# Kernel tuning notes

Hardware: AMD Instinct MI355X
Metric: run time of the kernel (lower is better)

## Reference

```python
import jax, jax.numpy as jnp
import numpy as np

DECAY = 0.2
TAU = float(-1.0 / np.log(DECAY))
THRESH = 0.5
DELAY = 0.1  # hidden spike events are scheduled at t + 0.1

B, E = 256, 1024
D_IN, D_H, D_OUT = 784, 400, 10
TIME_WINDOW = 64


def setup_inputs() -> dict:
    key = jax.random.key(0)
    k1, k2, k3, k4, k5, k6 = jax.random.split(key, 6)
    # chronologically sorted input spike event times per sample, in [0, time_window)
    event_times = jnp.sort(
        jax.random.uniform(k1, (B, E), dtype=jnp.float32) * TIME_WINDOW, axis=1
    )
    event_pixels = jax.random.randint(k2, (B, E), 0, D_IN, dtype=jnp.int32)
    W1 = jax.random.normal(k3, (D_H, D_IN), dtype=jnp.float32) * 0.1
    b1 = jax.random.normal(k4, (D_H,), dtype=jnp.float32) * 0.01
    W2 = jax.random.normal(k5, (D_OUT, D_H), dtype=jnp.float32) * 0.1
    b2 = jax.random.normal(k6, (D_OUT,), dtype=jnp.float32) * 0.01
    return {
        "event_times": event_times,
        "event_pixels": event_pixels,
        "W1": W1,
        "b1": b1,
        "W2": W2,
        "b2": b2,
        "time_window": TIME_WINDOW,
    }


def reference(event_times, event_pixels, W1, b1, W2, b2, time_window):
    # Event-driven LIF simulation, 784 -> 400 -> 10.
    # refractory_period == 0.0 in the source, so the refractory check never fires.
    Bn = event_times.shape[0]
    W1T = W1.T                               # [784, 400] for per-event gather
    bias1 = b1 / 784.0                       # bias contribution per input spike
    W2cols = W2.T + b2[None, :] / 400.0      # [400, 10] contribution per hidden spike
    tw = jnp.asarray(time_window, dtype=event_times.dtype)

    def hidden_event(carry, x):
        # Sequentially process one hidden neuron's (possible) spike within a
        # same-time group; resets can trigger mid-group so order matters.
        h2, counts = carry
        s, w = x                             # s: [B] bool, w: [10]
        mem_new = jnp.where(s[:, None], h2 + w[None, :], h2)
        f2 = s[:, None] & (mem_new >= THRESH)
        counts = counts + f2.astype(h2.dtype)
        h2 = jnp.where(f2, jnp.zeros_like(h2), mem_new)
        return (h2, counts), None

    def step(carry, x):
        h1, h2, counts, t1_prev, t2_prev = carry
        t, p = x                             # t: [B] float, p: [B] int
        # layer 1: decay to current time, integrate input spike, fire & reset
        h1 = h1 * jnp.exp(-(t - t1_prev) / TAU)[:, None] + W1T[p] + bias1[None, :]
        fired = h1 >= THRESH                 # [B, 400]
        h1 = jnp.where(fired, jnp.zeros_like(h1), h1)
        # layer 2: hidden events of this group all occur at t + DELAY
        th = t + DELAY
        h2 = h2 * jnp.exp(-(th - t2_prev) / TAU)[:, None]
        (h2, counts), _ = jax.lax.scan(hidden_event, (h2, counts), (fired.T, W2cols))
        return (h1, h2, counts, t, th), None

    f32 = event_times.dtype
    init = (
        jnp.zeros((Bn, 400), f32),           # h1_mem
        jnp.zeros((Bn, 10), f32),            # h2_mem
        jnp.zeros((Bn, 10), f32),            # h2_spike_counts
        jnp.zeros((Bn,), f32),               # h1 last update time
        jnp.zeros((Bn,), f32),               # h2 last update time
    )
    xs = (event_times.T, event_pixels.T)     # scan over E events chronologically
    (_, _, counts, _, _), _ = jax.lax.scan(step, init, xs)
    return counts / tw                       # [B, 10] rate-coded output
```

## Files before the change

### kernel.cpp

```cpp
#include <hip/hip_runtime.h>

#define CH 32
#define NCHUNK 32
#define NE 1024
#define DH 400
#define DIN 784
#define PF 8

#define TAUF ((float)0.6213349345596119)

__global__ void prep_transpose(const float* __restrict__ W1, float* __restrict__ W1T) {
  int idx = blockIdx.x * 256 + threadIdx.x;
  const int total = DIN * DH;
  if (idx < total) {
    int p = idx / DH;
    int j = idx - p * DH;
    W1T[idx] = W1[j * DIN + p];
  } else if (idx < total + 64) {
    W1T[idx] = 0.0f;
  }
}

#define STEP(WV)                                   \
  do {                                             \
    float mn_ = __fadd_rn(h2, (WV));               \
    bool f_ = (mn_ >= 0.5f);                       \
    cntf = f_ ? (cntf + 1.0f) : cntf;              \
    h2 = f_ ? 0.0f : mn_;                          \
  } while (0)

#define SPEC8(W0, W1, W2, W3, W4, W5, W6, W7)                                  \
  do {                                                                         \
    float q0f = __fadd_rn(h2, (W0));                                           \
    float q1f = __fadd_rn(q0f, (W1));                                          \
    float q2f = __fadd_rn(q1f, (W2));                                          \
    float q3f = __fadd_rn(q2f, (W3));                                          \
    float q4f = __fadd_rn(q3f, (W4));                                          \
    float q5f = __fadd_rn(q4f, (W5));                                          \
    float q6f = __fadd_rn(q5f, (W6));                                          \
    float q7f = __fadd_rn(q6f, (W7));                                          \
    bool anyF = (q0f >= 0.5f) | (q1f >= 0.5f) | (q2f >= 0.5f) | (q3f >= 0.5f) |\
                (q4f >= 0.5f) | (q5f >= 0.5f) | (q6f >= 0.5f) | (q7f >= 0.5f); \
    if (!anyF) {                                                               \
      h2 = q7f;                                                                \
    } else {                                                                   \
      STEP(W0); STEP(W1); STEP(W2); STEP(W3);                                  \
      STEP(W4); STEP(W5); STEP(W6); STEP(W7);                                  \
    }                                                                          \
  } while (0)

#define WSEL(PW, CW, WB)                            \
  do {                                              \
    bool c_ = (N >= (PW));                          \
    q = c_ ? (CW) : q;                              \
    r = c_ ? (N - (PW)) : r;                        \
    wb = c_ ? (WB) : wb;                            \
  } while (0)

#define RSEL64()                                                               \
  unsigned lo = (unsigned)q, hi = (unsigned)(q >> 32);                         \
  unsigned pc = (unsigned)__popc(lo);                                          \
  bool gg = r >= pc; unsigned base = gg ? 32u : 0u;                            \
  unsigned x = gg ? hi : lo; r = gg ? r - pc : r;                              \
  pc = (unsigned)__popc(x & 0xFFFFu); gg = r >= pc; base += gg ? 16u : 0u;     \
  x = gg ? (x >> 16) : (x & 0xFFFFu); r = gg ? r - pc : r;                     \
  pc = (unsigned)__popc(x & 0xFFu); gg = r >= pc; base += gg ? 8u : 0u;        \
  x = gg ? (x >> 8) : (x & 0xFFu); r = gg ? r - pc : r;                        \
  pc = (unsigned)__popc(x & 0xFu); gg = r >= pc; base += gg ? 4u : 0u;         \
  x = gg ? (x >> 4) : (x & 0xFu); r = gg ? r - pc : r;                         \
  pc = (unsigned)__popc(x & 0x3u); gg = r >= pc; base += gg ? 2u : 0u;         \
  x = gg ? (x >> 2) : (x & 0x3u); r = gg ? r - pc : r;                         \
  gg = r >= (x & 1u); base += gg ? 1u : 0u;

template <bool TR>
__global__ __launch_bounds__(512, 2) void snn_main(
    const float* __restrict__ ET, const int* __restrict__ EP,
    const float* __restrict__ W1x, const float* __restrict__ b1,
    const float* __restrict__ W2, const float* __restrict__ b2,
    float* __restrict__ out) {
  __shared__ float s_W2c[401 * 16];
  __shared__ unsigned long long s_masks[3][CH][8];
  __shared__ float s_dec1[NE];
  __shared__ float s_dec2[NE];
  __shared__ int s_EP[NE];
  __shared__ __align__(16) int s_spklist[2][CH][64];
  __shared__ float s_wlist[2][CH][256];
  __shared__ int s_spkcnt[2][CH];
  __shared__ __align__(16) int s_spk2[64];

  const int tid = threadIdx.x;
  const int b = blockIdx.x;
  const int eb = b * NE;

  for (int i = tid; i < 401 * 16; i += 512) {
    int row = i >> 4, col = i & 15;
    float v = 0.0f;
    if (row < DH && col < 10) v = __fadd_rn(W2[col * DH + row], __fdiv_rn(b2[col], 400.0f));
    s_W2c[i] = v;
  }
  for (int i = tid; i < NE; i += 512) {
    s_EP[i] = EP[eb + i];
    float t = ET[eb + i];
    float tp = (i > 0) ? ET[eb + i - 1] : 0.0f;
    s_dec1[i] = expf(__fdiv_rn(-(t - tp), TAUF));
    float th = __fadd_rn(t, 0.1f);
    float thp = (i > 0) ? __fadd_rn(tp, 0.1f) : 0.0f;
    s_dec2[i] = expf(__fdiv_rn(-(th - thp), TAUF));
  }

  const bool isProd = (tid < 448);
  const int lane = tid & 63;
  const int wv = tid >> 6;
  const bool act = (tid < DH);

  float m1 = 0.0f;
  float b1v = act ? __fdiv_rn(b1[tid < DH ? tid : DH - 1], 784.0f) : 0.0f;
  float wp[PF];
  int pnP[PF];

  float h2 = 0.0f, cntf = 0.0f;
  const int kk = lane & 15;

  __syncthreads();

  if (isProd) {
#pragma unroll
    for (int i = 0; i < PF; ++i) {
      int p = s_EP[i];
      wp[i] = TR ? W1x[p * DH + tid] : W1x[(tid < DH ? tid : DH - 1) * DIN + p];
      pnP[i] = s_EP[i + PF];
    }
  } else {
#pragma unroll
    for (int i = 0; i < PF; ++i) { wp[i] = 0.0f; pnP[i] = 0; }
  }

  for (int it = 0; it <= NCHUNK + 1; ++it) {
    if (isProd) {
      if (it < NCHUNK) {
        const int mb = it % 3;
        const int gbase = it * CH;
#pragma unroll
        for (int e = 0; e < CH; ++e) {
          const int g = gbase + e;
          const int s = e & (PF - 1);
          float mm = __fmul_rn(m1, s_dec1[g]);
          mm = __fadd_rn(mm, wp[s]);
          mm = __fadd_rn(mm, b1v);
          bool fired = act && (mm >= 0.5f);
          unsigned long long bal = __ballot(fired);
          m1 = fired ? 0.0f : mm;
          if (lane == 0) s_masks[mb][e][wv] = bal;
          int pn = pnP[s];
          wp[s] = TR ? W1x[pn * DH + tid] : W1x[(tid < DH ? tid : DH - 1) * DIN + pn];
          pnP[s] = s_EP[(g + 2 * PF) & (NE - 1)];
        }
      }
      if (it >= 1 && it <= NCHUNK) {
        const int c = it - 1;
        const int mb = c % 3;
        const int lb = c & 1;
        for (int e = wv; e < CH; e += 7) {
          unsigned long long c0 = s_masks[mb][e][0];
          unsigned long long c1 = s_masks[mb][e][1];
          unsigned long long c2 = s_masks[mb][e][2];
          unsigned long long c3 = s_masks[mb][e][3];
          unsigned long long c4 = s_masks[mb][e][4];
          unsigned long long c5 = s_masks[mb][e][5];
          unsigned long long c6 = s_masks[mb][e][6];
          unsigned P1 = (unsigned)__popcll(c0);
          unsigned P2 = P1 + (unsigned)__popcll(c1);
          unsigned P3 = P2 + (unsigned)__popcll(c2);
          unsigned P4 = P3 + (unsigned)__popcll(c3);
          unsigned P5 = P4 + (unsigned)__popcll(c4);
          unsigned P6 = P5 + (unsigned)__popcll(c5);
          unsigned total = P6 + (unsigned)__popcll(c6);
          unsigned N = (unsigned)lane;
          unsigned long long q = c0;
          unsigned r = N, wb = 0;
          WSEL(P1, c1, 64);  WSEL(P2, c2, 128); WSEL(P3, c3, 192);
          WSEL(P4, c4, 256); WSEL(P5, c5, 320); WSEL(P6, c6, 384);
          RSEL64();
          int j = (int)(wb + base);
          j = (N < total) ? j : DH;
          s_spklist[lb][e][lane] = j;
          if (lane == 0) s_spkcnt[lb][e] = (int)total;
#pragma unroll
          for (int p = 0; p < 4; ++p) {
            int sl = p * 4 + (lane >> 4);
            int js = __builtin_amdgcn_ds_bpermute(sl << 2, j);
            float w = s_W2c[js * 16 + (lane & 15)];
            s_wlist[lb][e][sl * 16 + (lane & 15)] = w;
          }
        }
      }
    } else {
      if (it >= 2) {
        const int c = it - 2;
        const int lb = c & 1;
        const int mb = c % 3;
        const int gb2 = c * CH;

        auto loadEvt = [&](int ee, int& tot, float& cdv, float (&w)[16]) {
          tot = s_spkcnt[lb][ee];
          cdv = s_dec2[gb2 + ee];
#pragma unroll
          for (int i = 0; i < 16; ++i) w[i] = s_wlist[lb][ee][i * 16 + kk];
        };
        auto procEvt = [&](int e, int tot, float cdv, float (&w)[16]) {
          h2 = __fmul_rn(h2, cdv);
          if (tot > 0) {
            SPEC8(w[0], w[1], w[2], w[3], w[4], w[5], w[6], w[7]);
            if (tot > 8) {
              SPEC8(w[8], w[9], w[10], w[11], w[12], w[13], w[14], w[15]);
            }
            if (tot > 16) {
              int lim = tot < 64 ? tot : 64;
              for (int dn = 16; dn < lim; dn += 8) {
                const int4* sp = (const int4*)(&s_spklist[lb][e][dn]);
                int4 ja = sp[0], jb = sp[1];
                float v0 = s_W2c[ja.x * 16 + kk];
                float v1 = s_W2c[ja.y * 16 + kk];
                float v2 = s_W2c[ja.z * 16 + kk];
                float v3 = s_W2c[ja.w * 16 + kk];
                float v4 = s_W2c[jb.x * 16 + kk];
                float v5 = s_W2c[jb.y * 16 + kk];
                float v6 = s_W2c[jb.z * 16 + kk];
                float v7 = s_W2c[jb.w * 16 + kk];
                SPEC8(v0, v1, v2, v3, v4, v5, v6, v7);
              }
              if (tot > 64) {
                unsigned long long c0 = s_masks[mb][e][0];
                unsigned long long c1 = s_masks[mb][e][1];
                unsigned long long c2 = s_masks[mb][e][2];
                unsigned long long c3 = s_masks[mb][e][3];
                unsigned long long c4 = s_masks[mb][e][4];
                unsigned long long c5 = s_masks[mb][e][5];
                unsigned long long c6 = s_masks[mb][e][6];
                unsigned P1 = (unsigned)__popcll(c0);
                unsigned P2 = P1 + (unsigned)__popcll(c1);
                unsigned P3 = P2 + (unsigned)__popcll(c2);
                unsigned P4 = P3 + (unsigned)__popcll(c3);
                unsigned P5 = P4 + (unsigned)__popcll(c4);
                unsigned P6 = P5 + (unsigned)__popcll(c5);
                for (int done = 64; done < tot; done += 64) {
                  unsigned N = (unsigned)(done + lane);
                  unsigned long long q = c0;
                  unsigned r = N, wb = 0;
                  WSEL(P1, c1, 64);  WSEL(P2, c2, 128); WSEL(P3, c3, 192);
                  WSEL(P4, c4, 256); WSEL(P5, c5, 320); WSEL(P6, c6, 384);
                  RSEL64();
                  int j = (int)(wb + base);
                  j = (N < (unsigned)tot) ? j : DH;
                  s_spk2[lane] = j;
                  int cnt = tot - done; cnt = cnt > 64 ? 64 : cnt;
                  int nb2 = (cnt + 7) >> 3;
                  for (int bb = 0; bb < nb2; ++bb) {
                    const int4* sp = (const int4*)(s_spk2 + bb * 8);
                    int4 ja = sp[0], jb = sp[1];
                    float v0 = s_W2c[ja.x * 16 + kk];
                    float v1 = s_W2c[ja.y * 16 + kk];
                    float v2 = s_W2c[ja.z * 16 + kk];
                    float v3 = s_W2c[ja.w * 16 + kk];
                    float v4 = s_W2c[jb.x * 16 + kk];
                    float v5 = s_W2c[jb.y * 16 + kk];
                    float v6 = s_W2c[jb.z * 16 + kk];
                    float v7 = s_W2c[jb.w * 16 + kk];
                    SPEC8(v0, v1, v2, v3, v4, v5, v6, v7);
                  }
                }
              }
            }
          }
        };

        int totA, totB; float cdA, cdB; float wA[16], wB[16];
        loadEvt(0, totA, cdA, wA);
        for (int e = 0; e < CH; e += 2) {
          loadEvt(e + 1, totB, cdB, wB);
          procEvt(e, totA, cdA, wA);
          if (e + 2 < CH) loadEvt(e + 2, totA, cdA, wA);
          procEvt(e + 1, totB, cdB, wB);
        }
      }
    }
    __syncthreads();
  }

  if (!isProd && lane < 10) out[b * 10 + lane] = __fmul_rn(cntf, 0.015625f);
}

extern "C" void kernel_launch(void* const* d_in, const int* in_sizes, int n_in,
                              void* d_out, int out_size, void* d_ws, size_t ws_size,
                              hipStream_t stream) {
  const float* ET = (const float*)d_in[0];
  const int* EP = (const int*)d_in[1];
  const float* W1 = (const float*)d_in[2];
  const float* b1 = (const float*)d_in[3];
  const float* W2 = (const float*)d_in[4];
  const float* b2 = (const float*)d_in[5];
  float* out = (float*)d_out;

  const size_t need = (size_t)(DIN * DH + 64) * sizeof(float);
  if (ws_size >= need) {
    float* W1T = (float*)d_ws;
    hipLaunchKernelGGL(prep_transpose, dim3((DIN * DH + 64 + 255) / 256), dim3(256), 0, stream,
                       W1, W1T);
    hipLaunchKernelGGL((snn_main<true>), dim3(256), dim3(512), 0, stream,
                       ET, EP, W1T, b1, W2, b2, out);
  } else {
    hipLaunchKernelGGL((snn_main<false>), dim3(256), dim3(512), 0, stream,
                       ET, EP, W1, b1, W2, b2, out);
  }
}
```

Baseline: 253.4 us.

## Transpose mask and weight-list LDS layouts and broadcast per-event scalars via readlane

The producer loop now loads a chunk's decay factors and next pixel indices once per wave as vectors and extracts each per-event value with readlane, replacing per-event LDS loads. Ballot masks are written in pairs into a transposed [wave][event] layout, and the compactor reads all seven masks with one vector load plus readlanes. The weight list is transposed and padded so the consumer wave reads it with float4 loads, and the upper eight slots are built and read only when more than eight hidden neurons fired. The aim is fewer LDS instructions on the serial per-event path, at the cost of more scalar readlane traffic and conditional branches.

```diff
diff --git a/kernel.cpp b/kernel.cpp
--- a/kernel.cpp
+++ b/kernel.cpp
@@ -72,6 +72,10 @@
   x = gg ? (x >> 2) : (x & 0x3u); r = gg ? r - pc : r;                         \
   gg = r >= (x & 1u); base += gg ? 1u : 0u;
 
+__device__ __forceinline__ float rl_f(float v, int l) {
+  return __int_as_float(__builtin_amdgcn_readlane(__float_as_int(v), l));
+}
+
 template <bool TR>
 __global__ __launch_bounds__(512, 2) void snn_main(
     const float* __restrict__ ET, const int* __restrict__ EP,
@@ -79,12 +83,12 @@
     const float* __restrict__ W2, const float* __restrict__ b2,
     float* __restrict__ out) {
   __shared__ float s_W2c[401 * 16];
-  __shared__ unsigned long long s_masks[3][CH][8];
+  __shared__ __align__(16) unsigned long long s_masksT[3][8][CH + 2];
   __shared__ float s_dec1[NE];
   __shared__ float s_dec2[NE];
   __shared__ int s_EP[NE];
   __shared__ __align__(16) int s_spklist[2][CH][64];
-  __shared__ float s_wlist[2][CH][256];
+  __shared__ __align__(16) float s_wlistT[2][CH][16 * 20];
   __shared__ int s_spkcnt[2][CH];
   __shared__ __align__(16) int s_spk2[64];
 
@@ -116,7 +120,6 @@
   float m1 = 0.0f;
   float b1v = act ? __fdiv_rn(b1[tid < DH ? tid : DH - 1], 784.0f) : 0.0f;
   float wp[PF];
-  int pnP[PF];
 
   float h2 = 0.0f, cntf = 0.0f;
   const int kk = lane & 15;
@@ -128,11 +131,10 @@
     for (int i = 0; i < PF; ++i) {
       int p = s_EP[i];
       wp[i] = TR ? W1x[p * DH + tid] : W1x[(tid < DH ? tid : DH - 1) * DIN + p];
-      pnP[i] = s_EP[i + PF];
     }
   } else {
 #pragma unroll
-    for (int i = 0; i < PF; ++i) { wp[i] = 0.0f; pnP[i] = 0; }
+    for (int i = 0; i < PF; ++i) wp[i] = 0.0f;
   }
 
   for (int it = 0; it <= NCHUNK + 1; ++it) {
@@ -140,20 +142,27 @@
       if (it < NCHUNK) {
         const int mb = it % 3;
         const int gbase = it * CH;
+        float decv = s_dec1[(gbase + lane) & (NE - 1)];
+        int epv = s_EP[(gbase + 8 + lane) & (NE - 1)];
+        unsigned long long balPrev = 0ull;
 #pragma unroll
         for (int e = 0; e < CH; ++e) {
-          const int g = gbase + e;
-          const int s = e & (PF - 1);
-          float mm = __fmul_rn(m1, s_dec1[g]);
-          mm = __fadd_rn(mm, wp[s]);
+          float dv = rl_f(decv, e);
+          float mm = __fmul_rn(m1, dv);
+          mm = __fadd_rn(mm, wp[e & (PF - 1)]);
           mm = __fadd_rn(mm, b1v);
           bool fired = act && (mm >= 0.5f);
           unsigned long long bal = __ballot(fired);
           m1 = fired ? 0.0f : mm;
-          if (lane == 0) s_masks[mb][e][wv] = bal;
-          int pn = pnP[s];
-          wp[s] = TR ? W1x[pn * DH + tid] : W1x[(tid < DH ? tid : DH - 1) * DIN + pn];
-          pnP[s] = s_EP[(g + 2 * PF) & (NE - 1)];
+          if ((e & 1) == 0) {
+            balPrev = bal;
+          } else if (lane == 0) {
+            ulonglong2 pr; pr.x = balPrev; pr.y = bal;
+            *reinterpret_cast<ulonglong2*>(&s_masksT[mb][wv][e - 1]) = pr;
+          }
+          int pn = __builtin_amdgcn_readlane(epv, e);
+          wp[e & (PF - 1)] =
+              TR ? W1x[pn * DH + tid] : W1x[(tid < DH ? tid : DH - 1) * DIN + pn];
         }
       }
       if (it >= 1 && it <= NCHUNK) {
@@ -161,13 +170,28 @@
         const int mb = c % 3;
         const int lb = c & 1;
         for (int e = wv; e < CH; e += 7) {
-          unsigned long long c0 = s_masks[mb][e][0];
-          unsigned long long c1 = s_masks[mb][e][1];
-          unsigned long long c2 = s_masks[mb][e][2];
-          unsigned long long c3 = s_masks[mb][e][3];
-          unsigned long long c4 = s_masks[mb][e][4];
-          unsigned long long c5 = s_masks[mb][e][5];
-          unsigned long long c6 = s_masks[mb][e][6];
+          uint2 mw = *reinterpret_cast<const uint2*>(&s_masksT[mb][lane & 7][e]);
+          unsigned long long c0 =
+              ((unsigned long long)(unsigned)__builtin_amdgcn_readlane(mw.y, 0) << 32) |
+              (unsigned)__builtin_amdgcn_readlane(mw.x, 0);
+          unsigned long long c1 =
+              ((unsigned long long)(unsigned)__builtin_amdgcn_readlane(mw.y, 1) << 32) |
+              (unsigned)__builtin_amdgcn_readlane(mw.x, 1);
+          unsigned long long c2 =
+              ((unsigned long long)(unsigned)__builtin_amdgcn_readlane(mw.y, 2) << 32) |
+              (unsigned)__builtin_amdgcn_readlane(mw.x, 2);
+          unsigned long long c3 =
+              ((unsigned long long)(unsigned)__builtin_amdgcn_readlane(mw.y, 3) << 32) |
+              (unsigned)__builtin_amdgcn_readlane(mw.x, 3);
+          unsigned long long c4 =
+              ((unsigned long long)(unsigned)__builtin_amdgcn_readlane(mw.y, 4) << 32) |
+              (unsigned)__builtin_amdgcn_readlane(mw.x, 4);
+          unsigned long long c5 =
+              ((unsigned long long)(unsigned)__builtin_amdgcn_readlane(mw.y, 5) << 32) |
+              (unsigned)__builtin_amdgcn_readlane(mw.x, 5);
+          unsigned long long c6 =
+              ((unsigned long long)(unsigned)__builtin_amdgcn_readlane(mw.y, 6) << 32) |
+              (unsigned)__builtin_amdgcn_readlane(mw.x, 6);
           unsigned P1 = (unsigned)__popcll(c0);
           unsigned P2 = P1 + (unsigned)__popcll(c1);
           unsigned P3 = P2 + (unsigned)__popcll(c2);
@@ -186,11 +210,20 @@
           s_spklist[lb][e][lane] = j;
           if (lane == 0) s_spkcnt[lb][e] = (int)total;
 #pragma unroll
-          for (int p = 0; p < 4; ++p) {
+          for (int p = 0; p < 2; ++p) {
             int sl = p * 4 + (lane >> 4);
             int js = __builtin_amdgcn_ds_bpermute(sl << 2, j);
             float w = s_W2c[js * 16 + (lane & 15)];
-            s_wlist[lb][e][sl * 16 + (lane & 15)] = w;
+            s_wlistT[lb][e][(lane & 15) * 20 + sl] = w;
+          }
+          if (total > 8) {
+#pragma unroll
+            for (int p = 2; p < 4; ++p) {
+              int sl = p * 4 + (lane >> 4);
+              int js = __builtin_amdgcn_ds_bpermute(sl << 2, j);
+              float w = s_W2c[js * 16 + (lane & 15)];
+              s_wlistT[lb][e][(lane & 15) * 20 + sl] = w;
+            }
           }
         }
       }
@@ -200,12 +233,21 @@
         const int lb = c & 1;
         const int mb = c % 3;
         const int gb2 = c * CH;
+        int cntv = s_spkcnt[lb][lane & 31];
+        float d2v = s_dec2[gb2 + (lane & 31)];
 
         auto loadEvt = [&](int ee, int& tot, float& cdv, float (&w)[16]) {
-          tot = s_spkcnt[lb][ee];
-          cdv = s_dec2[gb2 + ee];
-#pragma unroll
-          for (int i = 0; i < 16; ++i) w[i] = s_wlist[lb][ee][i * 16 + kk];
+          tot = __builtin_amdgcn_readlane(cntv, ee);
+          cdv = rl_f(d2v, ee);
+          const float4* wrow = reinterpret_cast<const float4*>(&s_wlistT[lb][ee][kk * 20]);
+          float4 a = wrow[0], b4 = wrow[1];
+          w[0] = a.x; w[1] = a.y; w[2] = a.z; w[3] = a.w;
+          w[4] = b4.x; w[5] = b4.y; w[6] = b4.z; w[7] = b4.w;
+          if (tot > 8) {
+            float4 c4 = wrow[2], d4 = wrow[3];
+            w[8] = c4.x; w[9] = c4.y; w[10] = c4.z; w[11] = c4.w;
+            w[12] = d4.x; w[13] = d4.y; w[14] = d4.z; w[15] = d4.w;
+          }
         };
         auto procEvt = [&](int e, int tot, float cdv, float (&w)[16]) {
           h2 = __fmul_rn(h2, cdv);
@@ -230,13 +272,28 @@
                 SPEC8(v0, v1, v2, v3, v4, v5, v6, v7);
               }
               if (tot > 64) {
-                unsigned long long c0 = s_masks[mb][e][0];
-                unsigned long long c1 = s_masks[mb][e][1];
-                unsigned long long c2 = s_masks[mb][e][2];
-                unsigned long long c3 = s_masks[mb][e][3];
-                unsigned long long c4 = s_masks[mb][e][4];
-                unsigned long long c5 = s_masks[mb][e][5];
-                unsigned long long c6 = s_masks[mb][e][6];
+                uint2 mw = *reinterpret_cast<const uint2*>(&s_masksT[mb][lane & 7][e]);
+                unsigned long long c0 =
+                    ((unsigned long long)(unsigned)__builtin_amdgcn_readlane(mw.y, 0) << 32) |
+                    (unsigned)__builtin_amdgcn_readlane(mw.x, 0);
+                unsigned long long c1 =
+                    ((unsigned long long)(unsigned)__builtin_amdgcn_readlane(mw.y, 1) << 32) |
+                    (unsigned)__builtin_amdgcn_readlane(mw.x, 1);
+                unsigned long long c2 =
+                    ((unsigned long long)(unsigned)__builtin_amdgcn_readlane(mw.y, 2) << 32) |
+                    (unsigned)__builtin_amdgcn_readlane(mw.x, 2);
+                unsigned long long c3 =
+                    ((unsigned long long)(unsigned)__builtin_amdgcn_readlane(mw.y, 3) << 32) |
+                    (unsigned)__builtin_amdgcn_readlane(mw.x, 3);
+                unsigned long long c4 =
+                    ((unsigned long long)(unsigned)__builtin_amdgcn_readlane(mw.y, 4) << 32) |
+                    (unsigned)__builtin_amdgcn_readlane(mw.x, 4);
+                unsigned long long c5 =
+                    ((unsigned long long)(unsigned)__builtin_amdgcn_readlane(mw.y, 5) << 32) |
+                    (unsigned)__builtin_amdgcn_readlane(mw.x, 5);
+                unsigned long long c6 =
+                    ((unsigned long long)(unsigned)__builtin_amdgcn_readlane(mw.y, 6) << 32) |
+                    (unsigned)__builtin_amdgcn_readlane(mw.x, 6);
                 unsigned P1 = (unsigned)__popcll(c0);
                 unsigned P2 = P1 + (unsigned)__popcll(c1);
                 unsigned P3 = P2 + (unsigned)__popcll(c2);
```

Measured after the change: 244.7 us. 3.4% less time.
